# Optimization experiments

Hardware: AMD Instinct MI355X
Metric: run time of the kernel (lower is better)

Reference implementation:

```python
import jax, jax.numpy as jnp
import numpy as np

HIDDEN = 1024
GMM = 16


def setup_inputs() -> dict:
    key = jax.random.key(0)
    ks = jax.random.split(key, 9)
    B, T, D, S = 16, 1024, HIDDEN, 512
    sc_ih = 1.0 / np.sqrt(2 * D)
    sc_hh = 1.0 / np.sqrt(D)
    return {
        "input_h_c": jax.random.normal(ks[0], (B, T, D), jnp.float32),
        "memory": jax.random.normal(ks[1], (B, S, D), jnp.float32),
        "input_lengths": jax.random.randint(ks[2], (B,), 1, S + 1),
        "W_ih": jax.random.uniform(ks[3], (4 * D, 2 * D), jnp.float32, -sc_ih, sc_ih),
        "W_hh": jax.random.uniform(ks[4], (4 * D, D), jnp.float32, -sc_hh, sc_hh),
        "b_ih": jax.random.uniform(ks[5], (4 * D,), jnp.float32, -sc_hh, sc_hh),
        "b_hh": jax.random.uniform(ks[6], (4 * D,), jnp.float32, -sc_hh, sc_hh),
        "Wg_w": jax.random.uniform(ks[7], (3 * GMM, D), jnp.float32, -sc_hh, sc_hh),
        "Wg_b": jax.random.uniform(ks[8], (3 * GMM,), jnp.float32, -sc_hh, sc_hh),
    }


def reference(input_h_c, memory, input_lengths, W_ih, W_hh, b_ih, b_hh, Wg_w, Wg_b):
    B, T, D = input_h_c.shape
    S = memory.shape[1]
    M = Wg_b.shape[0] // 3
    b = b_ih + b_hh
    u = jnp.arange(S, dtype=input_h_c.dtype)  # positions u

    def step(carry, x_t):
        h, c, ctx = carry
        x = jnp.concatenate([x_t, ctx], axis=-1)  # [B, 2D]
        gates = x @ W_ih.T + h @ W_hh.T + b  # [B, 4D], torch gate order i,f,g,o
        i_g, f_g, g_g, o_g = jnp.split(gates, 4, axis=-1)
        c = jax.nn.sigmoid(f_g) * c + jax.nn.sigmoid(i_g) * jnp.tanh(g_g)
        h = jax.nn.sigmoid(o_g) * jnp.tanh(c)
        phi = h @ Wg_w.T + Wg_b  # [B, 3M]
        ksi = jnp.exp(phi[:, :M])
        beta = jnp.exp(phi[:, M:2 * M])
        alpha = jax.nn.softmax(phi[:, 2 * M:], axis=-1)
        # 1/(1+exp((ksi-u)/beta)) == sigmoid((u-ksi)/beta)
        z = (u[None, None, :] - ksi[:, :, None]) / beta[:, :, None]  # [B,M,S]
        half = 0.5 / beta[:, :, None]
        F_R = jax.nn.sigmoid(z + half)  # CDF at u+0.5
        F_L = jax.nn.sigmoid(z - half)  # CDF at u-0.5
        w = jnp.einsum('bm,bms->bs', alpha, F_R - F_L)  # [B,S]
        term = 1.0 - jnp.einsum('bm,bms->bs', alpha, F_R)  # [B,S]
        ctx = jnp.einsum('bs,bsd->bd', w, memory)  # [B,D]
        return (h, c, ctx), (w, term)

    h0 = jnp.zeros((B, D), input_h_c.dtype)
    c0 = jnp.zeros((B, D), input_h_c.dtype)
    ctx0 = jnp.zeros((B, D), input_h_c.dtype)
    (h, c, ctx), (ws, terms) = jax.lax.scan(
        step, (h0, c0, ctx0), jnp.swapaxes(input_h_c, 0, 1))
    alignment = jnp.swapaxes(ws, 0, 1)  # [B,T,S]
    term_last = terms[-1]  # [B,S]
    termination = jnp.take_along_axis(term_last, (input_lengths - 1)[:, None], axis=1)  # [B,1]
    context = ctx[:, None, :]  # [B,1,D], last-step context (as returned by torch forward)
    return (context, alignment, termination)
```

## Files before the change

kernel.cpp:

```cpp
#include <hip/hip_runtime.h>
#include <hip/hip_fp16.h>

#define BB 16
#define TT 1024
#define DD 1024
#define SS 512
#define KK 3072

#define NBLK 256
#define NTHR 512

#define OUT_ALIGN 16384
#define OUT_TERM  8404992

typedef __attribute__((ext_vector_type(8))) short short8;
typedef __attribute__((ext_vector_type(4))) float floatx4;
typedef __attribute__((ext_vector_type(2))) _Float16 half2v;

struct KParams {
  const float* x;
  const float* mem;
  const int*   lens;
  const float* W_ih;
  const float* W_hh;
  const float* b_ih;
  const float* b_hh;
  const float* Wg_w;
  const float* Wg_b;
  float* out;
  unsigned* bar;
  unsigned short* xc0;
  unsigned short* xc1;
  unsigned* wgbf;
};

__device__ __forceinline__ float sigf(float v) {
  return __builtin_amdgcn_rcpf(1.0f + __expf(-v));
}
__device__ __forceinline__ float tanhfast(float v) {
  float a = fabsf(v);
  float e = __expf(-2.0f * a);
  float r = (1.0f - e) * __builtin_amdgcn_rcpf(1.0f + e);
  return v < 0.0f ? -r : r;
}

__device__ __forceinline__ unsigned short f2bf(float f) {
  unsigned u = __float_as_uint(f);
  return (unsigned short)((u + 0x7FFFu + ((u >> 16) & 1u)) >> 16);
}
__device__ __forceinline__ float bf2f(unsigned short h) {
  return __uint_as_float(((unsigned)h) << 16);
}
__device__ __forceinline__ unsigned pack2bf(float a, float b) {
  return (unsigned)f2bf(a) | ((unsigned)f2bf(b) << 16);
}

__device__ __forceinline__ void cstore_u32(unsigned* p2, unsigned v) {
  __hip_atomic_store(p2, v, __ATOMIC_RELAXED, __HIP_MEMORY_SCOPE_AGENT);
}
__device__ __forceinline__ unsigned cload_u32(const unsigned* p2) {
  return __hip_atomic_load(p2, __ATOMIC_RELAXED, __HIP_MEMORY_SCOPE_AGENT);
}
__device__ __forceinline__ unsigned long long cload_u64(const unsigned long long* p2) {
  return __hip_atomic_load(p2, __ATOMIC_RELAXED, __HIP_MEMORY_SCOPE_AGENT);
}

__device__ __forceinline__ void lds_barrier() {
  asm volatile("s_waitcnt lgkmcnt(0)\n\ts_barrier" ::: "memory");
}

__device__ __forceinline__ void grid_barrier(unsigned* bar, unsigned ep, int blk) {
  __syncthreads();
  if (threadIdx.x == 0) cstore_u32(&bar[64 + blk * 32], ep);
  if (threadIdx.x < NBLK) {
    while (cload_u32(&bar[64 + threadIdx.x * 32]) < ep) __builtin_amdgcn_s_sleep(1);
  }
  __syncthreads();
}

union UF { unsigned long long u[2]; short8 s; };
struct AF8 { UF f[8]; };

__device__ __forceinline__ void xh_load(const unsigned short* xc, int ab, AF8& A) {
  const unsigned long long* xb = (const unsigned long long*)xc + ab;
#pragma unroll
  for (int s2 = 0; s2 < 4; ++s2) {
    A.f[s2].u[0]     = cload_u64(xb + s2 * 8);
    A.f[s2].u[1]     = cload_u64(xb + s2 * 8 + 1);
    A.f[4 + s2].u[0] = cload_u64(xb + 512 + s2 * 8);
    A.f[4 + s2].u[1] = cload_u64(xb + 512 + s2 * 8 + 1);
  }
}
__device__ __forceinline__ void xh_mfma(const AF8& A, const short8* bfr,
                                        floatx4& A0, floatx4& A1) {
  floatx4 a0 = {0.f, 0.f, 0.f, 0.f}, a1 = {0.f, 0.f, 0.f, 0.f};
#pragma unroll
  for (int s2 = 0; s2 < 4; s2 += 2) {
    a0 = __builtin_amdgcn_mfma_f32_16x16x32_bf16(A.f[s2].s,     bfr[s2],     a0, 0, 0, 0);
    a1 = __builtin_amdgcn_mfma_f32_16x16x32_bf16(A.f[s2 + 1].s, bfr[s2 + 1], a1, 0, 0, 0);
    a0 = __builtin_amdgcn_mfma_f32_16x16x32_bf16(A.f[4 + s2].s,     bfr[8 + s2],     a0, 0, 0, 0);
    a1 = __builtin_amdgcn_mfma_f32_16x16x32_bf16(A.f[4 + s2 + 1].s, bfr[8 + s2 + 1], a1, 0, 0, 0);
  }
  A0 = a0; A1 = a1;
}

__global__ __launch_bounds__(NTHR, 2) void tts_kernel(KParams p) {
  extern __shared__ char smem[];
  half2v* memsh2 = (half2v*)smem;

  __shared__ float redC[8 * 4 * 65 + 4];
  __shared__ unsigned hshu[8 * 65];
  __shared__ float php[384];
  __shared__ float alsh[16], ksish[16], invbsh[16];
  __shared__ float Rsh[513];
  __shared__ half2v wsh2[256];
  __shared__ float ctxp[8][64];
  __shared__ float bsh48[48];

  const int t    = threadIdx.x;
  const int blk  = blockIdx.x;
  const int lane = t & 63;
  const int w    = t >> 6;
  const int bbt  = blk & 15;
  const int dc   = blk >> 4;

  short8 bfr[12];
  {
    const int n = lane & 15;
    const int r = (n & 3) * 1024 + blk * 4 + (n >> 2);
    const int q = lane >> 4;
#pragma unroll
    for (int ki = 0; ki < 12; ++ki) {
      short8 v;
      const int k0 = (ki >> 2) * 1024 + w * 128 + (ki & 3) * 32 + q * 8;
#pragma unroll
      for (int j = 0; j < 8; ++j) {
        int k = k0 + j;
        float wv = (k < 2048) ? p.W_ih[(size_t)r * 2048 + k]
                              : p.W_hh[(size_t)r * 1024 + (k - 2048)];
        v[j] = (short)f2bf(wv);
      }
      bfr[ki] = v;
    }
  }
  float biasreg[4] = {0.f, 0.f, 0.f, 0.f};
  if (t < 64) {
    int dl = t & 3;
#pragma unroll
    for (int g = 0; g < 4; ++g) {
      int r = g * 1024 + blk * 4 + dl;
      biasreg[g] = p.b_ih[r] + p.b_hh[r];
    }
  }
  if (t < 48) bsh48[t] = p.Wg_b[t];
  {
    int dl = t & 63, sp = t >> 6;
    for (int pr = sp; pr < 256; pr += 8) {
      const float* mp = p.mem + (size_t)bbt * SS * DD + (size_t)(2 * pr) * DD + dc * 64 + dl;
      half2v v;
      v.x = (_Float16)mp[0];
      v.y = (_Float16)mp[DD];
      memsh2[pr * 64 + dl] = v;
    }
  }
  if (t < 32) {
    int k = dc * 64 + 2 * t;
    const float* xs = p.x + (size_t)bbt * TT * DD + k;
    cstore_u32((unsigned*)(p.xc0 + bbt * KK + k), pack2bf(xs[0], xs[1]));
    cstore_u32((unsigned*)(p.xc0 + bbt * KK + 1024 + k), 0u);
    cstore_u32((unsigned*)(p.xc0 + bbt * KK + 2048 + k), 0u);
  }
  if (blk == 0) {
    for (int i = t; i < 48 * 512; i += NTHR)
      cstore_u32(&p.wgbf[i], pack2bf(p.Wg_w[2 * i], p.Wg_w[2 * i + 1]));
  }

  float c_val = 0.0f;
  unsigned ep = 0;
  unsigned short* xc_cur = p.xc0;
  unsigned short* xc_nxt = p.xc1;
  const int ab = ((lane & 15) * KK + w * 128 + (lane >> 4) * 8) >> 2;

  grid_barrier(p.bar, ++ep, blk);

  floatx4 accXH0, accXH1;
  {
    AF8 a;
    xh_load(xc_cur, ab, a);
    xh_mfma(a, bfr, accXH0, accXH1);
  }

  for (int tstep = 0; tstep < TT; ++tstep) {
    {
      const unsigned long long* xb = (const unsigned long long*)xc_cur + ab;
      UF afc[4];
#pragma unroll
      for (int s2 = 0; s2 < 4; ++s2) {
        afc[s2].u[0] = cload_u64(xb + 256 + s2 * 8);
        afc[s2].u[1] = cload_u64(xb + 256 + s2 * 8 + 1);
      }
      floatx4 a0 = accXH0, a1 = accXH1;
      a0 = __builtin_amdgcn_mfma_f32_16x16x32_bf16(afc[0].s, bfr[4], a0, 0, 0, 0);
      a1 = __builtin_amdgcn_mfma_f32_16x16x32_bf16(afc[1].s, bfr[5], a1, 0, 0, 0);
      a0 = __builtin_amdgcn_mfma_f32_16x16x32_bf16(afc[2].s, bfr[6], a0, 0, 0, 0);
      a1 = __builtin_amdgcn_mfma_f32_16x16x32_bf16(afc[3].s, bfr[7], a1, 0, 0, 0);
      a0 += a1;
#pragma unroll
      for (int reg = 0; reg < 4; ++reg)
        redC[(w * 4 + reg) * 65 + lane] = a0[reg];
    }
    lds_barrier();
    if (t < 64) {
      int b = t >> 2, dl = t & 3;
      float gate[4];
#pragma unroll
      for (int g = 0; g < 4; ++g) {
        int ls = (b >> 2) * 16 + (dl * 4 + g);
        float s = biasreg[g];
#pragma unroll
        for (int w2 = 0; w2 < 8; ++w2) s += redC[(w2 * 4 + (b & 3)) * 65 + ls];
        gate[g] = s;
      }
      c_val = sigf(gate[1]) * c_val + sigf(gate[0]) * tanhfast(gate[2]);
      float hv = sigf(gate[3]) * tanhfast(c_val);
      float hn = __shfl_down(hv, 1, 64);
      if ((t & 1) == 0)
        cstore_u32((unsigned*)(xc_nxt + b * KK + 2048 + blk * 4 + dl), pack2bf(hv, hn));
    } else if (t < 96) {
      if (tstep + 1 < TT) {
        int k = dc * 64 + 2 * (t - 64);
        const float* xs = p.x + (size_t)bbt * TT * DD + (size_t)(tstep + 1) * DD + k;
        cstore_u32((unsigned*)(xc_nxt + bbt * KK + k), pack2bf(xs[0], xs[1]));
      }
    }
    grid_barrier(p.bar, ++ep, blk);

    unsigned hword = cload_u32((const unsigned*)(xc_nxt + bbt * KK + 2048) + t);
    AF8 afx;
    xh_load(xc_nxt, ab, afx);
    hshu[(t >> 6) * 65 + (t & 63)] = hword;
    lds_barrier();
    if (t < 384) {
      int m = t >> 3, part = t & 7;
      const unsigned* wgp = p.wgbf + m * 512 + part * 64;
      const unsigned* hrow = hshu + part * 65;
      float s0 = 0.f, s1 = 0.f, s2 = 0.f, s3 = 0.f;
#pragma unroll 4
      for (int i = 0; i < 64; i += 4) {
        unsigned u0 = hrow[i],     g0 = wgp[i];
        unsigned u1 = hrow[i + 1], g1 = wgp[i + 1];
        unsigned u2 = hrow[i + 2], g2 = wgp[i + 2];
        unsigned u3 = hrow[i + 3], g3 = wgp[i + 3];
        s0 += bf2f((unsigned short)u0) * bf2f((unsigned short)g0)
            + bf2f((unsigned short)(u0 >> 16)) * bf2f((unsigned short)(g0 >> 16));
        s1 += bf2f((unsigned short)u1) * bf2f((unsigned short)g1)
            + bf2f((unsigned short)(u1 >> 16)) * bf2f((unsigned short)(g1 >> 16));
        s2 += bf2f((unsigned short)u2) * bf2f((unsigned short)g2)
            + bf2f((unsigned short)(u2 >> 16)) * bf2f((unsigned short)(g2 >> 16));
        s3 += bf2f((unsigned short)u3) * bf2f((unsigned short)g3)
            + bf2f((unsigned short)(u3 >> 16)) * bf2f((unsigned short)(g3 >> 16));
      }
      php[t] = (s0 + s1) + (s2 + s3);
    }
    lds_barrier();
    if (t < 64) {
      float s = 0.f;
      if (t < 48) {
        s = bsh48[t];
#pragma unroll
        for (int i = 0; i < 8; ++i) s += php[t * 8 + i];
      }
      float mx = s;
#pragma unroll
      for (int o = 1; o < 16; o <<= 1) mx = fmaxf(mx, __shfl_xor(mx, o, 64));
      float e = __expf(s - mx);
      float sm = e;
#pragma unroll
      for (int o = 1; o < 16; o <<= 1) sm += __shfl_xor(sm, o, 64);
      float alpha_v = e * __builtin_amdgcn_rcpf(sm);
      float ksi_v   = __expf(s);
      float invb_v  = __expf(-s);
      if (t >= 32) { if (t < 48) alsh[t - 32] = alpha_v; }
      else if (t < 16) ksish[t] = ksi_v;
      else invbsh[t - 16] = invb_v;
      int m = t & 15;
      float am = __shfl(alpha_v, 32 + m, 64);
      float km = __shfl(ksi_v, m, 64);
      float bm = __shfl(invb_v, 16 + m, 64);
      float term = am * sigf((-0.5f - km) * bm);
#pragma unroll
      for (int o = 1; o < 16; o <<= 1) term += __shfl_xor(term, o, 64);
      if (t == 48) Rsh[0] = term;
    }
    lds_barrier();
    {
      float su = (float)t;
      float rv0 = 0.f, rv1 = 0.f;
#pragma unroll
      for (int m = 0; m < 16; m += 2) {
        rv0 += alsh[m]     * sigf((su + 0.5f - ksish[m])     * invbsh[m]);
        rv1 += alsh[m + 1] * sigf((su + 0.5f - ksish[m + 1]) * invbsh[m + 1]);
      }
      float rv = rv0 + rv1;
      float rvp = __shfl_up(rv, 1, 64);
      float rvn = __shfl_down(rv, 1, 64);
      Rsh[t + 1] = rv;
      if ((t & 1) == 0) {
        half2v v2;
        v2.x = (_Float16)(rv - rvp);
        v2.y = (_Float16)(rvn - rv);
        wsh2[t >> 1] = v2;
      }
      if (dc == 0 && (t & 63) != 0)
        p.out[OUT_ALIGN + ((size_t)bbt * TT + tstep) * SS + t] = rv - rvp;
    }
    lds_barrier();
    {
      if (dc == 0 && t < 8)
        p.out[OUT_ALIGN + ((size_t)bbt * TT + tstep) * SS + 64 * t] =
            Rsh[64 * t + 1] - Rsh[64 * t];
      if (tstep == TT - 1 && dc == 0 && t == 0)
        p.out[OUT_TERM + bbt] = 1.0f - Rsh[p.lens[bbt]];
      int dl = t & 63, sp = t >> 6;
      float b0 = Rsh[64 * sp], b1 = Rsh[64 * sp + 1], b2 = Rsh[64 * sp + 2];
      half2v w0;
      w0.x = (_Float16)(b1 - b0);
      w0.y = (_Float16)(b2 - b1);
      float s0 = __builtin_amdgcn_fdot2(memsh2[(sp * 32) * 64 + dl], w0, 0.f, false);
      float s1 = 0.f;
#pragma unroll
      for (int q = 1; q < 32; ++q) {
        int pr = sp * 32 + q;
        float v = __builtin_amdgcn_fdot2(memsh2[pr * 64 + dl], wsh2[pr],
                                         (q & 1) ? s1 : s0, false);
        if (q & 1) s1 = v; else s0 = v;
      }
      ctxp[sp][dl] = s0 + s1;
    }
    lds_barrier();
    if (t < 64) {
      float cv = 0.f;
#pragma unroll
      for (int pp = 0; pp < 8; ++pp) cv += ctxp[pp][t];
      if (tstep == TT - 1) p.out[bbt * DD + dc * 64 + t] = cv;
      float cvn = __shfl_down(cv, 1, 64);
      if ((t & 1) == 0)
        cstore_u32((unsigned*)(xc_nxt + bbt * KK + 1024 + dc * 64 + t), pack2bf(cv, cvn));
    }
    __builtin_amdgcn_sched_barrier(0);
    xh_mfma(afx, bfr, accXH0, accXH1);
    grid_barrier(p.bar, ++ep, blk);

    unsigned short* tmp = xc_cur; xc_cur = xc_nxt; xc_nxt = tmp;
  }
}

extern "C" void kernel_launch(void* const* d_in, const int* in_sizes, int n_in,
                              void* d_out, int out_size, void* d_ws, size_t ws_size,
                              hipStream_t stream) {
  (void)in_sizes; (void)n_in; (void)out_size; (void)ws_size;
  KParams p;
  p.x    = (const float*)d_in[0];
  p.mem  = (const float*)d_in[1];
  p.lens = (const int*)d_in[2];
  p.W_ih = (const float*)d_in[3];
  p.W_hh = (const float*)d_in[4];
  p.b_ih = (const float*)d_in[5];
  p.b_hh = (const float*)d_in[6];
  p.Wg_w = (const float*)d_in[7];
  p.Wg_b = (const float*)d_in[8];
  p.out  = (float*)d_out;
  p.bar  = (unsigned*)d_ws;
  p.xc0  = (unsigned short*)((char*)d_ws + 36864);
  p.xc1  = (unsigned short*)((char*)d_ws + 36864 + BB * KK * 2);
  p.wgbf = (unsigned*)((char*)d_ws + 36864 + 2 * BB * KK * 2);

  hipMemsetAsync(d_ws, 0, 36864, stream);

  const unsigned dynLds = 65536;
  hipFuncSetAttribute((const void*)tts_kernel, hipFuncAttributeMaxDynamicSharedMemorySize,
                      (int)dynLds);

  void* args[] = { &p };
  hipLaunchCooperativeKernel((const void*)tts_kernel, dim3(NBLK), dim3(NTHR), args, dynLds,
                             stream);
}
```

Measured before the change: 14.85 ms.

## Replace grid barriers with tagged per-word flag polling for X/H/C exchange

Removes the two per-step grid-wide barriers and instead packs each bf16 pair with a 32-bit step tag into a 64-bit word. Consumers poll the exact words they need until the tag matches, using double-buffered X/H/C arrays. The point is to let blocks proceed as soon as their inputs are ready instead of waiting on all 256 blocks. In exchange, global traffic doubles per exchanged element and spin polling is added on many loads. Buffer reuse across steps also depends on the tags for correctness.

```diff
diff --git a/kernel.cpp b/kernel.cpp
--- a/kernel.cpp
+++ b/kernel.cpp
@@ -5,7 +5,6 @@
 #define TT 1024
 #define DD 1024
 #define SS 512
-#define KK 3072
 
 #define NBLK 256
 #define NTHR 512
@@ -29,8 +28,9 @@
   const float* Wg_b;
   float* out;
   unsigned* bar;
-  unsigned short* xc0;
-  unsigned short* xc1;
+  unsigned long long* X;
+  unsigned long long* H;
+  unsigned long long* C;
   unsigned* wgbf;
 };
 
@@ -61,8 +61,14 @@
 __device__ __forceinline__ unsigned cload_u32(const unsigned* p2) {
   return __hip_atomic_load(p2, __ATOMIC_RELAXED, __HIP_MEMORY_SCOPE_AGENT);
 }
+__device__ __forceinline__ void cstore_u64(unsigned long long* p2, unsigned long long v) {
+  __hip_atomic_store(p2, v, __ATOMIC_RELAXED, __HIP_MEMORY_SCOPE_AGENT);
+}
 __device__ __forceinline__ unsigned long long cload_u64(const unsigned long long* p2) {
   return __hip_atomic_load(p2, __ATOMIC_RELAXED, __HIP_MEMORY_SCOPE_AGENT);
+}
+__device__ __forceinline__ unsigned long long tagpack(unsigned tag, unsigned data) {
+  return ((unsigned long long)tag << 32) | (unsigned long long)data;
 }
 
 __device__ __forceinline__ void lds_barrier() {
@@ -78,30 +84,28 @@
   __syncthreads();
 }
 
-union UF { unsigned long long u[2]; short8 s; };
-struct AF8 { UF f[8]; };
-
-__device__ __forceinline__ void xh_load(const unsigned short* xc, int ab, AF8& A) {
-  const unsigned long long* xb = (const unsigned long long*)xc + ab;
-#pragma unroll
-  for (int s2 = 0; s2 < 4; ++s2) {
-    A.f[s2].u[0]     = cload_u64(xb + s2 * 8);
-    A.f[s2].u[1]     = cload_u64(xb + s2 * 8 + 1);
-    A.f[4 + s2].u[0] = cload_u64(xb + 512 + s2 * 8);
-    A.f[4 + s2].u[1] = cload_u64(xb + 512 + s2 * 8 + 1);
-  }
-}
-__device__ __forceinline__ void xh_mfma(const AF8& A, const short8* bfr,
-                                        floatx4& A0, floatx4& A1) {
-  floatx4 a0 = {0.f, 0.f, 0.f, 0.f}, a1 = {0.f, 0.f, 0.f, 0.f};
-#pragma unroll
-  for (int s2 = 0; s2 < 4; s2 += 2) {
-    a0 = __builtin_amdgcn_mfma_f32_16x16x32_bf16(A.f[s2].s,     bfr[s2],     a0, 0, 0, 0);
-    a1 = __builtin_amdgcn_mfma_f32_16x16x32_bf16(A.f[s2 + 1].s, bfr[s2 + 1], a1, 0, 0, 0);
-    a0 = __builtin_amdgcn_mfma_f32_16x16x32_bf16(A.f[4 + s2].s,     bfr[8 + s2],     a0, 0, 0, 0);
-    a1 = __builtin_amdgcn_mfma_f32_16x16x32_bf16(A.f[4 + s2 + 1].s, bfr[8 + s2 + 1], a1, 0, 0, 0);
-  }
-  A0 = a0; A1 = a1;
+__device__ __forceinline__ void load16(const unsigned long long* b, unsigned long long* v) {
+#pragma unroll
+  for (int c = 0; c < 4; ++c)
+#pragma unroll
+    for (int j = 0; j < 4; ++j) v[c * 4 + j] = cload_u64(b + c * 16 + j);
+}
+__device__ __forceinline__ void poll16(const unsigned long long* b, unsigned long long* v,
+                                       unsigned want) {
+  for (;;) {
+    unsigned bad = 0;
+#pragma unroll
+    for (int i = 0; i < 16; ++i) bad |= ((unsigned)(v[i] >> 32)) ^ want;
+    if (!bad) return;
+    __builtin_amdgcn_s_sleep(1);
+    load16(b, v);
+  }
+}
+__device__ __forceinline__ short8 mk8(const unsigned long long* v) {
+  union { unsigned u[4]; short8 s; } pk;
+#pragma unroll
+  for (int j = 0; j < 4; ++j) pk.u[j] = (unsigned)v[j];
+  return pk.s;
 }
 
 __global__ __launch_bounds__(NTHR, 2) void tts_kernel(KParams p) {
@@ -164,46 +168,51 @@
     }
   }
   if (t < 32) {
-    int k = dc * 64 + 2 * t;
-    const float* xs = p.x + (size_t)bbt * TT * DD + k;
-    cstore_u32((unsigned*)(p.xc0 + bbt * KK + k), pack2bf(xs[0], xs[1]));
-    cstore_u32((unsigned*)(p.xc0 + bbt * KK + 1024 + k), 0u);
-    cstore_u32((unsigned*)(p.xc0 + bbt * KK + 2048 + k), 0u);
+    const float* xs = p.x + (size_t)bbt * TT * DD + dc * 64 + 2 * t;
+    cstore_u64(&p.X[bbt * 512 + dc * 32 + t], tagpack(1u, pack2bf(xs[0], xs[1])));
   }
   if (blk == 0) {
     for (int i = t; i < 48 * 512; i += NTHR)
       cstore_u32(&p.wgbf[i], pack2bf(p.Wg_w[2 * i], p.Wg_w[2 * i + 1]));
   }
+  grid_barrier(p.bar, 1u, blk);
 
   float c_val = 0.0f;
-  unsigned ep = 0;
-  unsigned short* xc_cur = p.xc0;
-  unsigned short* xc_nxt = p.xc1;
-  const int ab = ((lane & 15) * KK + w * 128 + (lane >> 4) * 8) >> 2;
-
-  grid_barrier(p.bar, ++ep, blk);
+  const int pab = (lane & 15) * 512 + w * 64 + (lane >> 4) * 4;
 
   floatx4 accXH0, accXH1;
   {
-    AF8 a;
-    xh_load(xc_cur, ab, a);
-    xh_mfma(a, bfr, accXH0, accXH1);
+    unsigned long long vx[16], vh[16];
+    const unsigned long long* xb = p.X + pab;
+    const unsigned long long* hb = p.H + 8192 + pab;
+    load16(xb, vx); load16(hb, vh);
+    poll16(xb, vx, 1u); poll16(hb, vh, 0u);
+    floatx4 b0 = {0.f,0.f,0.f,0.f}, b1 = {0.f,0.f,0.f,0.f};
+    b0 = __builtin_amdgcn_mfma_f32_16x16x32_bf16(mk8(vx + 0),  bfr[0],  b0, 0, 0, 0);
+    b1 = __builtin_amdgcn_mfma_f32_16x16x32_bf16(mk8(vx + 4),  bfr[1],  b1, 0, 0, 0);
+    b0 = __builtin_amdgcn_mfma_f32_16x16x32_bf16(mk8(vx + 8),  bfr[2],  b0, 0, 0, 0);
+    b1 = __builtin_amdgcn_mfma_f32_16x16x32_bf16(mk8(vx + 12), bfr[3],  b1, 0, 0, 0);
+    b0 = __builtin_amdgcn_mfma_f32_16x16x32_bf16(mk8(vh + 0),  bfr[8],  b0, 0, 0, 0);
+    b1 = __builtin_amdgcn_mfma_f32_16x16x32_bf16(mk8(vh + 4),  bfr[9],  b1, 0, 0, 0);
+    b0 = __builtin_amdgcn_mfma_f32_16x16x32_bf16(mk8(vh + 8),  bfr[10], b0, 0, 0, 0);
+    b1 = __builtin_amdgcn_mfma_f32_16x16x32_bf16(mk8(vh + 12), bfr[11], b1, 0, 0, 0);
+    accXH0 = b0; accXH1 = b1;
   }
 
   for (int tstep = 0; tstep < TT; ++tstep) {
+    const int q1 = tstep & 1;
+    const int q0 = q1 ^ 1;
+
     {
-      const unsigned long long* xb = (const unsigned long long*)xc_cur + ab;
-      UF afc[4];
-#pragma unroll
-      for (int s2 = 0; s2 < 4; ++s2) {
-        afc[s2].u[0] = cload_u64(xb + 256 + s2 * 8);
-        afc[s2].u[1] = cload_u64(xb + 256 + s2 * 8 + 1);
-      }
+      const unsigned long long* cb = p.C + q0 * 8192 + pab;
+      unsigned long long vc[16];
+      load16(cb, vc);
+      poll16(cb, vc, (unsigned)tstep);
       floatx4 a0 = accXH0, a1 = accXH1;
-      a0 = __builtin_amdgcn_mfma_f32_16x16x32_bf16(afc[0].s, bfr[4], a0, 0, 0, 0);
-      a1 = __builtin_amdgcn_mfma_f32_16x16x32_bf16(afc[1].s, bfr[5], a1, 0, 0, 0);
-      a0 = __builtin_amdgcn_mfma_f32_16x16x32_bf16(afc[2].s, bfr[6], a0, 0, 0, 0);
-      a1 = __builtin_amdgcn_mfma_f32_16x16x32_bf16(afc[3].s, bfr[7], a1, 0, 0, 0);
+      a0 = __builtin_amdgcn_mfma_f32_16x16x32_bf16(mk8(vc + 0),  bfr[4], a0, 0, 0, 0);
+      a1 = __builtin_amdgcn_mfma_f32_16x16x32_bf16(mk8(vc + 4),  bfr[5], a1, 0, 0, 0);
+      a0 = __builtin_amdgcn_mfma_f32_16x16x32_bf16(mk8(vc + 8),  bfr[6], a0, 0, 0, 0);
+      a1 = __builtin_amdgcn_mfma_f32_16x16x32_bf16(mk8(vc + 12), bfr[7], a1, 0, 0, 0);
       a0 += a1;
 #pragma unroll
       for (int reg = 0; reg < 4; ++reg)
@@ -224,21 +233,34 @@
       c_val = sigf(gate[1]) * c_val + sigf(gate[0]) * tanhfast(gate[2]);
       float hv = sigf(gate[3]) * tanhfast(c_val);
       float hn = __shfl_down(hv, 1, 64);
-      if ((t & 1) == 0)
-        cstore_u32((unsigned*)(xc_nxt + b * KK + 2048 + blk * 4 + dl), pack2bf(hv, hn));
+      if ((dl & 1) == 0)
+        cstore_u64(&p.H[q1 * 8192 + b * 512 + blk * 2 + (dl >> 1)],
+                   tagpack((unsigned)(tstep + 1), pack2bf(hv, hn)));
     } else if (t < 96) {
       if (tstep + 1 < TT) {
-        int k = dc * 64 + 2 * (t - 64);
-        const float* xs = p.x + (size_t)bbt * TT * DD + (size_t)(tstep + 1) * DD + k;
-        cstore_u32((unsigned*)(xc_nxt + bbt * KK + k), pack2bf(xs[0], xs[1]));
-      }
-    }
-    grid_barrier(p.bar, ++ep, blk);
-
-    unsigned hword = cload_u32((const unsigned*)(xc_nxt + bbt * KK + 2048) + t);
-    AF8 afx;
-    xh_load(xc_nxt, ab, afx);
-    hshu[(t >> 6) * 65 + (t & 63)] = hword;
+        const float* xs = p.x + (size_t)bbt * TT * DD + (size_t)(tstep + 1) * DD +
+                          dc * 64 + 2 * (t - 64);
+        cstore_u64(&p.X[q0 * 8192 + bbt * 512 + dc * 32 + (t - 64)],
+                   tagpack((unsigned)(tstep + 2), pack2bf(xs[0], xs[1])));
+      }
+    }
+
+    const unsigned wantH = (unsigned)(tstep + 1);
+    unsigned long long vx[16], vh[16];
+    const unsigned long long* xb = p.X + q0 * 8192 + pab;
+    const unsigned long long* hb = p.H + q1 * 8192 + pab;
+    if (tstep + 1 < TT) { load16(xb, vx); load16(hb, vh); }
+    __builtin_amdgcn_sched_barrier(0);
+    unsigned long long hv64;
+    {
+      const unsigned long long* hp = p.H + q1 * 8192 + bbt * 512 + t;
+      hv64 = cload_u64(hp);
+      while ((unsigned)(hv64 >> 32) != wantH) {
+        __builtin_amdgcn_s_sleep(1);
+        hv64 = cload_u64(hp);
+      }
+    }
+    hshu[(t >> 6) * 65 + (t & 63)] = (unsigned)hv64;
     lds_barrier();
     if (t < 384) {
       int m = t >> 3, part = t & 7;
@@ -345,13 +367,24 @@
       if (tstep == TT - 1) p.out[bbt * DD + dc * 64 + t] = cv;
       float cvn = __shfl_down(cv, 1, 64);
       if ((t & 1) == 0)
-        cstore_u32((unsigned*)(xc_nxt + bbt * KK + 1024 + dc * 64 + t), pack2bf(cv, cvn));
-    }
-    __builtin_amdgcn_sched_barrier(0);
-    xh_mfma(afx, bfr, accXH0, accXH1);
-    grid_barrier(p.bar, ++ep, blk);
-
-    unsigned short* tmp = xc_cur; xc_cur = xc_nxt; xc_nxt = tmp;
+        cstore_u64(&p.C[q1 * 8192 + bbt * 512 + dc * 32 + (t >> 1)],
+                   tagpack((unsigned)(tstep + 1), pack2bf(cv, cvn)));
+    }
+    if (tstep + 1 < TT) {
+      poll16(xb, vx, (unsigned)(tstep + 2));
+      poll16(hb, vh, wantH);
+      __builtin_amdgcn_sched_barrier(0);
+      floatx4 b0 = {0.f,0.f,0.f,0.f}, b1 = {0.f,0.f,0.f,0.f};
+      b0 = __builtin_amdgcn_mfma_f32_16x16x32_bf16(mk8(vx + 0),  bfr[0],  b0, 0, 0, 0);
+      b1 = __builtin_amdgcn_mfma_f32_16x16x32_bf16(mk8(vx + 4),  bfr[1],  b1, 0, 0, 0);
+      b0 = __builtin_amdgcn_mfma_f32_16x16x32_bf16(mk8(vx + 8),  bfr[2],  b0, 0, 0, 0);
+      b1 = __builtin_amdgcn_mfma_f32_16x16x32_bf16(mk8(vx + 12), bfr[3],  b1, 0, 0, 0);
+      b0 = __builtin_amdgcn_mfma_f32_16x16x32_bf16(mk8(vh + 0),  bfr[8],  b0, 0, 0, 0);
+      b1 = __builtin_amdgcn_mfma_f32_16x16x32_bf16(mk8(vh + 4),  bfr[9],  b1, 0, 0, 0);
+      b0 = __builtin_amdgcn_mfma_f32_16x16x32_bf16(mk8(vh + 8),  bfr[10], b0, 0, 0, 0);
+      b1 = __builtin_amdgcn_mfma_f32_16x16x32_bf16(mk8(vh + 12), bfr[11], b1, 0, 0, 0);
+      accXH0 = b0; accXH1 = b1;
+    }
   }
 }
 
@@ -371,11 +404,12 @@
   p.Wg_b = (const float*)d_in[8];
   p.out  = (float*)d_out;
   p.bar  = (unsigned*)d_ws;
-  p.xc0  = (unsigned short*)((char*)d_ws + 36864);
-  p.xc1  = (unsigned short*)((char*)d_ws + 36864 + BB * KK * 2);
-  p.wgbf = (unsigned*)((char*)d_ws + 36864 + 2 * BB * KK * 2);
-
-  hipMemsetAsync(d_ws, 0, 36864, stream);
+  p.X    = (unsigned long long*)((char*)d_ws + 36864);
+  p.H    = (unsigned long long*)((char*)d_ws + 36864 + 131072);
+  p.C    = (unsigned long long*)((char*)d_ws + 36864 + 262144);
+  p.wgbf = (unsigned*)((char*)d_ws + 36864 + 393216);
+
+  hipMemsetAsync(d_ws, 0, 36864 + 393216, stream);
 
   const unsigned dynLds = 65536;
   hipFuncSetAttribute((const void*)tts_kernel, hipFuncAttributeMaxDynamicSharedMemorySize,
```

New measurement: 25.01 ms. 1.68x slower.

## Halve block count, double per-block tile, read x directly from global

Applied to the files above, without the earlier changes.

Reduces the cooperative grid from 256 to 128 blocks. Each block now owns 8 hidden units (two N-tiles of MFMA) and 128 context columns, with twice the memory slice in LDS (128KB dynamic). The input x is no longer staged through the shared bf16 exchange buffer. Each wave loads it straight from global memory and converts it with v_cvt_pk_bf16_f32, which shrinks the exchange buffer to ctx+h. The grid barrier polling is adapted to 128 blocks. The goal is lower grid-barrier and cross-block traffic cost per timestep, at the price of more per-block work, register pressure and LDS use.

```diff
diff --git a/kernel.cpp b/kernel.cpp
--- a/kernel.cpp
+++ b/kernel.cpp
@@ -5,9 +5,9 @@
 #define TT 1024
 #define DD 1024
 #define SS 512
-#define KK 3072
-
-#define NBLK 256
+#define KK2 2048
+
+#define NBLK 128
 #define NTHR 512
 
 #define OUT_ALIGN 16384
@@ -54,6 +54,11 @@
 __device__ __forceinline__ unsigned pack2bf(float a, float b) {
   return (unsigned)f2bf(a) | ((unsigned)f2bf(b) << 16);
 }
+__device__ __forceinline__ unsigned cvtpk(float a, float b) {
+  unsigned r;
+  asm volatile("v_cvt_pk_bf16_f32 %0, %1, %2" : "=v"(r) : "v"(a), "v"(b));
+  return r;
+}
 
 __device__ __forceinline__ void cstore_u32(unsigned* p2, unsigned v) {
   __hip_atomic_store(p2, v, __ATOMIC_RELAXED, __HIP_MEMORY_SCOPE_AGENT);
@@ -72,49 +77,43 @@
 __device__ __forceinline__ void grid_barrier(unsigned* bar, unsigned ep, int blk) {
   __syncthreads();
   if (threadIdx.x == 0) cstore_u32(&bar[64 + blk * 32], ep);
-  if (threadIdx.x < NBLK) {
-    while (cload_u32(&bar[64 + threadIdx.x * 32]) < ep) __builtin_amdgcn_s_sleep(1);
+  if (threadIdx.x < 64) {
+    while (cload_u32(&bar[64 + (int)threadIdx.x * 32]) < ep) __builtin_amdgcn_s_sleep(1);
+    while (cload_u32(&bar[64 + ((int)threadIdx.x + 64) * 32]) < ep) __builtin_amdgcn_s_sleep(1);
   }
   __syncthreads();
 }
 
-union UF { unsigned long long u[2]; short8 s; };
-struct AF8 { UF f[8]; };
-
-__device__ __forceinline__ void xh_load(const unsigned short* xc, int ab, AF8& A) {
-  const unsigned long long* xb = (const unsigned long long*)xc + ab;
-#pragma unroll
-  for (int s2 = 0; s2 < 4; ++s2) {
-    A.f[s2].u[0]     = cload_u64(xb + s2 * 8);
-    A.f[s2].u[1]     = cload_u64(xb + s2 * 8 + 1);
-    A.f[4 + s2].u[0] = cload_u64(xb + 512 + s2 * 8);
-    A.f[4 + s2].u[1] = cload_u64(xb + 512 + s2 * 8 + 1);
-  }
-}
-__device__ __forceinline__ void xh_mfma(const AF8& A, const short8* bfr,
-                                        floatx4& A0, floatx4& A1) {
-  floatx4 a0 = {0.f, 0.f, 0.f, 0.f}, a1 = {0.f, 0.f, 0.f, 0.f};
-#pragma unroll
-  for (int s2 = 0; s2 < 4; s2 += 2) {
-    a0 = __builtin_amdgcn_mfma_f32_16x16x32_bf16(A.f[s2].s,     bfr[s2],     a0, 0, 0, 0);
-    a1 = __builtin_amdgcn_mfma_f32_16x16x32_bf16(A.f[s2 + 1].s, bfr[s2 + 1], a1, 0, 0, 0);
-    a0 = __builtin_amdgcn_mfma_f32_16x16x32_bf16(A.f[4 + s2].s,     bfr[8 + s2],     a0, 0, 0, 0);
-    a1 = __builtin_amdgcn_mfma_f32_16x16x32_bf16(A.f[4 + s2 + 1].s, bfr[8 + s2 + 1], a1, 0, 0, 0);
-  }
-  A0 = a0; A1 = a1;
+union UF { unsigned w[4]; unsigned long long u[2]; short8 s; };
+
+#define MFMA16 __builtin_amdgcn_mfma_f32_16x16x32_bf16
+
+__device__ __forceinline__ void xh_mfma(const UF* xf, const UF* hf, const short8* bfr,
+                                        floatx4& a00, floatx4& a01,
+                                        floatx4& a10, floatx4& a11) {
+  floatx4 z = {0.f, 0.f, 0.f, 0.f};
+  a00 = z; a01 = z; a10 = z; a11 = z;
+  a00 = MFMA16(xf[0].s, bfr[0],  a00, 0, 0, 0); a01 = MFMA16(xf[1].s, bfr[1],  a01, 0, 0, 0);
+  a10 = MFMA16(xf[0].s, bfr[12], a10, 0, 0, 0); a11 = MFMA16(xf[1].s, bfr[13], a11, 0, 0, 0);
+  a00 = MFMA16(xf[2].s, bfr[2],  a00, 0, 0, 0); a01 = MFMA16(xf[3].s, bfr[3],  a01, 0, 0, 0);
+  a10 = MFMA16(xf[2].s, bfr[14], a10, 0, 0, 0); a11 = MFMA16(xf[3].s, bfr[15], a11, 0, 0, 0);
+  a00 = MFMA16(hf[0].s, bfr[8],  a00, 0, 0, 0); a01 = MFMA16(hf[1].s, bfr[9],  a01, 0, 0, 0);
+  a10 = MFMA16(hf[0].s, bfr[20], a10, 0, 0, 0); a11 = MFMA16(hf[1].s, bfr[21], a11, 0, 0, 0);
+  a00 = MFMA16(hf[2].s, bfr[10], a00, 0, 0, 0); a01 = MFMA16(hf[3].s, bfr[11], a01, 0, 0, 0);
+  a10 = MFMA16(hf[2].s, bfr[22], a10, 0, 0, 0); a11 = MFMA16(hf[3].s, bfr[23], a11, 0, 0, 0);
 }
 
 __global__ __launch_bounds__(NTHR, 2) void tts_kernel(KParams p) {
   extern __shared__ char smem[];
   half2v* memsh2 = (half2v*)smem;
 
-  __shared__ float redC[8 * 4 * 65 + 4];
+  __shared__ float redC[64 * 65 + 4];
   __shared__ unsigned hshu[8 * 65];
   __shared__ float php[384];
   __shared__ float alsh[16], ksish[16], invbsh[16];
   __shared__ float Rsh[513];
   __shared__ half2v wsh2[256];
-  __shared__ float ctxp[8][64];
+  __shared__ float ctxp[4][128];
   __shared__ float bsh48[48];
 
   const int t    = threadIdx.x;
@@ -124,121 +123,145 @@
   const int bbt  = blk & 15;
   const int dc   = blk >> 4;
 
-  short8 bfr[12];
+  short8 bfr[24];
   {
     const int n = lane & 15;
-    const int r = (n & 3) * 1024 + blk * 4 + (n >> 2);
     const int q = lane >> 4;
 #pragma unroll
-    for (int ki = 0; ki < 12; ++ki) {
-      short8 v;
-      const int k0 = (ki >> 2) * 1024 + w * 128 + (ki & 3) * 32 + q * 8;
-#pragma unroll
-      for (int j = 0; j < 8; ++j) {
-        int k = k0 + j;
-        float wv = (k < 2048) ? p.W_ih[(size_t)r * 2048 + k]
-                              : p.W_hh[(size_t)r * 1024 + (k - 2048)];
-        v[j] = (short)f2bf(wv);
-      }
-      bfr[ki] = v;
+    for (int nt = 0; nt < 2; ++nt) {
+      const int r = (n & 3) * 1024 + blk * 8 + nt * 4 + (n >> 2);
+#pragma unroll
+      for (int ki = 0; ki < 12; ++ki) {
+        short8 v;
+        const int k0 = (ki >> 2) * 1024 + w * 128 + (ki & 3) * 32 + q * 8;
+#pragma unroll
+        for (int j = 0; j < 8; ++j) {
+          int k = k0 + j;
+          float wv = (k < 2048) ? p.W_ih[(size_t)r * 2048 + k]
+                                : p.W_hh[(size_t)r * 1024 + (k - 2048)];
+          v[j] = (short)f2bf(wv);
+        }
+        bfr[nt * 12 + ki] = v;
+      }
     }
   }
   float biasreg[4] = {0.f, 0.f, 0.f, 0.f};
-  if (t < 64) {
-    int dl = t & 3;
+  if (t < 128) {
+    int dl = t & 7;
 #pragma unroll
     for (int g = 0; g < 4; ++g) {
-      int r = g * 1024 + blk * 4 + dl;
+      int r = g * 1024 + blk * 8 + dl;
       biasreg[g] = p.b_ih[r] + p.b_hh[r];
     }
   }
   if (t < 48) bsh48[t] = p.Wg_b[t];
   {
-    int dl = t & 63, sp = t >> 6;
-    for (int pr = sp; pr < 256; pr += 8) {
-      const float* mp = p.mem + (size_t)bbt * SS * DD + (size_t)(2 * pr) * DD + dc * 64 + dl;
+    int dl = t & 127, sp = t >> 7;
+    for (int pr = sp; pr < 256; pr += 4) {
+      const float* mp = p.mem + (size_t)bbt * SS * DD + (size_t)(2 * pr) * DD + dc * 128 + dl;
       half2v v;
       v.x = (_Float16)mp[0];
       v.y = (_Float16)mp[DD];
-      memsh2[pr * 64 + dl] = v;
-    }
-  }
-  if (t < 32) {
-    int k = dc * 64 + 2 * t;
-    const float* xs = p.x + (size_t)bbt * TT * DD + k;
-    cstore_u32((unsigned*)(p.xc0 + bbt * KK + k), pack2bf(xs[0], xs[1]));
-    cstore_u32((unsigned*)(p.xc0 + bbt * KK + 1024 + k), 0u);
-    cstore_u32((unsigned*)(p.xc0 + bbt * KK + 2048 + k), 0u);
+      memsh2[pr * 128 + dl] = v;
+    }
   }
   if (blk == 0) {
     for (int i = t; i < 48 * 512; i += NTHR)
       cstore_u32(&p.wgbf[i], pack2bf(p.Wg_w[2 * i], p.Wg_w[2 * i + 1]));
   }
+  grid_barrier(p.bar, 1u, blk);
 
   float c_val = 0.0f;
-  unsigned ep = 0;
+  unsigned ep = 1;
   unsigned short* xc_cur = p.xc0;
   unsigned short* xc_nxt = p.xc1;
-  const int ab = ((lane & 15) * KK + w * 128 + (lane >> 4) * 8) >> 2;
-
-  grid_barrier(p.bar, ++ep, blk);
-
-  floatx4 accXH0, accXH1;
+  const int ab2 = ((lane & 15) * KK2 + w * 128 + ((lane >> 4) * 8)) >> 2;
+  const float* xrow = p.x + (size_t)(lane & 15) * TT * DD + w * 128 + ((lane >> 4) * 8);
+
+  floatx4 acc00, acc01, acc10, acc11;
   {
-    AF8 a;
-    xh_load(xc_cur, ab, a);
-    xh_mfma(a, bfr, accXH0, accXH1);
+    UF xf[4], hf[4];
+#pragma unroll
+    for (int sub = 0; sub < 4; ++sub) {
+      floatx4 lo = *(const floatx4*)(xrow + sub * 32);
+      floatx4 hi = *(const floatx4*)(xrow + sub * 32 + 4);
+      xf[sub].w[0] = cvtpk(lo[0], lo[1]); xf[sub].w[1] = cvtpk(lo[2], lo[3]);
+      xf[sub].w[2] = cvtpk(hi[0], hi[1]); xf[sub].w[3] = cvtpk(hi[2], hi[3]);
+    }
+    const unsigned long long* hb = (const unsigned long long*)p.xc0 + ab2 + 256;
+#pragma unroll
+    for (int sub = 0; sub < 4; ++sub) {
+      hf[sub].u[0] = cload_u64(hb + sub * 8);
+      hf[sub].u[1] = cload_u64(hb + sub * 8 + 1);
+    }
+    xh_mfma(xf, hf, bfr, acc00, acc01, acc10, acc11);
   }
 
   for (int tstep = 0; tstep < TT; ++tstep) {
     {
-      const unsigned long long* xb = (const unsigned long long*)xc_cur + ab;
-      UF afc[4];
-#pragma unroll
-      for (int s2 = 0; s2 < 4; ++s2) {
-        afc[s2].u[0] = cload_u64(xb + 256 + s2 * 8);
-        afc[s2].u[1] = cload_u64(xb + 256 + s2 * 8 + 1);
-      }
-      floatx4 a0 = accXH0, a1 = accXH1;
-      a0 = __builtin_amdgcn_mfma_f32_16x16x32_bf16(afc[0].s, bfr[4], a0, 0, 0, 0);
-      a1 = __builtin_amdgcn_mfma_f32_16x16x32_bf16(afc[1].s, bfr[5], a1, 0, 0, 0);
-      a0 = __builtin_amdgcn_mfma_f32_16x16x32_bf16(afc[2].s, bfr[6], a0, 0, 0, 0);
-      a1 = __builtin_amdgcn_mfma_f32_16x16x32_bf16(afc[3].s, bfr[7], a1, 0, 0, 0);
-      a0 += a1;
-#pragma unroll
-      for (int reg = 0; reg < 4; ++reg)
-        redC[(w * 4 + reg) * 65 + lane] = a0[reg];
-    }
-    lds_barrier();
-    if (t < 64) {
-      int b = t >> 2, dl = t & 3;
+      const unsigned long long* cb = (const unsigned long long*)xc_cur + ab2;
+      UF fc[4];
+#pragma unroll
+      for (int sub = 0; sub < 4; ++sub) {
+        fc[sub].u[0] = cload_u64(cb + sub * 8);
+        fc[sub].u[1] = cload_u64(cb + sub * 8 + 1);
+      }
+      floatx4 c00 = acc00, c01 = acc01, c10 = acc10, c11 = acc11;
+      c00 = MFMA16(fc[0].s, bfr[4],  c00, 0, 0, 0); c01 = MFMA16(fc[1].s, bfr[5],  c01, 0, 0, 0);
+      c10 = MFMA16(fc[0].s, bfr[16], c10, 0, 0, 0); c11 = MFMA16(fc[1].s, bfr[17], c11, 0, 0, 0);
+      c00 = MFMA16(fc[2].s, bfr[6],  c00, 0, 0, 0); c01 = MFMA16(fc[3].s, bfr[7],  c01, 0, 0, 0);
+      c10 = MFMA16(fc[2].s, bfr[18], c10, 0, 0, 0); c11 = MFMA16(fc[3].s, bfr[19], c11, 0, 0, 0);
+      c00 += c01; c10 += c11;
+#pragma unroll
+      for (int reg = 0; reg < 4; ++reg) {
+        redC[(w * 8 + reg) * 65 + lane]     = c00[reg];
+        redC[(w * 8 + 4 + reg) * 65 + lane] = c10[reg];
+      }
+    }
+    lds_barrier();
+    if (t < 128) {
+      int b = t >> 3, dl = t & 7, nt = dl >> 2, dl4 = dl & 3;
+      int row = nt * 4 + (b & 3);
       float gate[4];
 #pragma unroll
       for (int g = 0; g < 4; ++g) {
-        int ls = (b >> 2) * 16 + (dl * 4 + g);
+        int ls = ((b >> 2) << 4) | (dl4 * 4 + g);
         float s = biasreg[g];
 #pragma unroll
-        for (int w2 = 0; w2 < 8; ++w2) s += redC[(w2 * 4 + (b & 3)) * 65 + ls];
+        for (int w2 = 0; w2 < 8; ++w2) s += redC[(w2 * 8 + row) * 65 + ls];
         gate[g] = s;
       }
       c_val = sigf(gate[1]) * c_val + sigf(gate[0]) * tanhfast(gate[2]);
       float hv = sigf(gate[3]) * tanhfast(c_val);
       float hn = __shfl_down(hv, 1, 64);
       if ((t & 1) == 0)
-        cstore_u32((unsigned*)(xc_nxt + b * KK + 2048 + blk * 4 + dl), pack2bf(hv, hn));
-    } else if (t < 96) {
-      if (tstep + 1 < TT) {
-        int k = dc * 64 + 2 * (t - 64);
-        const float* xs = p.x + (size_t)bbt * TT * DD + (size_t)(tstep + 1) * DD + k;
-        cstore_u32((unsigned*)(xc_nxt + bbt * KK + k), pack2bf(xs[0], xs[1]));
-      }
+        cstore_u32((unsigned*)(xc_nxt + b * KK2 + 1024 + blk * 8 + dl), pack2bf(hv, hn));
     }
     grid_barrier(p.bar, ++ep, blk);
 
-    unsigned hword = cload_u32((const unsigned*)(xc_nxt + bbt * KK + 2048) + t);
-    AF8 afx;
-    xh_load(xc_nxt, ab, afx);
-    hshu[(t >> 6) * 65 + (t & 63)] = hword;
+    unsigned long long hword = 0;
+    if (t < 256) hword = cload_u64((const unsigned long long*)xc_nxt + bbt * 512 + 256 + t);
+    UF hf[4];
+    floatx4 xlo[4], xhi[4];
+    if (tstep + 1 < TT) {
+      const unsigned long long* hb = (const unsigned long long*)xc_nxt + ab2 + 256;
+#pragma unroll
+      for (int sub = 0; sub < 4; ++sub) {
+        hf[sub].u[0] = cload_u64(hb + sub * 8);
+        hf[sub].u[1] = cload_u64(hb + sub * 8 + 1);
+      }
+      const float* xp = xrow + (size_t)(tstep + 1) * DD;
+#pragma unroll
+      for (int sub = 0; sub < 4; ++sub) {
+        xlo[sub] = *(const floatx4*)(xp + sub * 32);
+        xhi[sub] = *(const floatx4*)(xp + sub * 32 + 4);
+      }
+    }
+    if (t < 256) {
+      int row = t >> 5, col = (t & 31) * 2;
+      hshu[row * 65 + col]     = (unsigned)hword;
+      hshu[row * 65 + col + 1] = (unsigned)(hword >> 32);
+    }
     lds_barrier();
     if (t < 384) {
       int m = t >> 3, part = t & 7;
@@ -321,34 +344,39 @@
             Rsh[64 * t + 1] - Rsh[64 * t];
       if (tstep == TT - 1 && dc == 0 && t == 0)
         p.out[OUT_TERM + bbt] = 1.0f - Rsh[p.lens[bbt]];
-      int dl = t & 63, sp = t >> 6;
-      float b0 = Rsh[64 * sp], b1 = Rsh[64 * sp + 1], b2 = Rsh[64 * sp + 2];
-      half2v w0;
-      w0.x = (_Float16)(b1 - b0);
-      w0.y = (_Float16)(b2 - b1);
-      float s0 = __builtin_amdgcn_fdot2(memsh2[(sp * 32) * 64 + dl], w0, 0.f, false);
-      float s1 = 0.f;
-#pragma unroll
+      int dl = t & 127, sp = t >> 7;
+      const int pb = sp * 64;
+      half2v wa = wsh2[pb];       wa.x = (_Float16)(Rsh[2 * pb + 1] - Rsh[2 * pb]);
+      half2v wb = wsh2[pb + 32];  wb.x = (_Float16)(Rsh[2 * pb + 65] - Rsh[2 * pb + 64]);
+      float s0 = __builtin_amdgcn_fdot2(memsh2[pb * 128 + dl], wa, 0.f, false);
+      float s1 = __builtin_amdgcn_fdot2(memsh2[(pb + 32) * 128 + dl], wb, 0.f, false);
+#pragma unroll 8
       for (int q = 1; q < 32; ++q) {
-        int pr = sp * 32 + q;
-        float v = __builtin_amdgcn_fdot2(memsh2[pr * 64 + dl], wsh2[pr],
-                                         (q & 1) ? s1 : s0, false);
-        if (q & 1) s1 = v; else s0 = v;
+        s0 = __builtin_amdgcn_fdot2(memsh2[(pb + q) * 128 + dl],      wsh2[pb + q],      s0, false);
+        s1 = __builtin_amdgcn_fdot2(memsh2[(pb + 32 + q) * 128 + dl], wsh2[pb + 32 + q], s1, false);
       }
       ctxp[sp][dl] = s0 + s1;
     }
     lds_barrier();
-    if (t < 64) {
-      float cv = 0.f;
-#pragma unroll
-      for (int pp = 0; pp < 8; ++pp) cv += ctxp[pp][t];
-      if (tstep == TT - 1) p.out[bbt * DD + dc * 64 + t] = cv;
+    if (t < 128) {
+      float cv = ctxp[0][t] + ctxp[1][t] + ctxp[2][t] + ctxp[3][t];
+      if (tstep == TT - 1) p.out[bbt * DD + dc * 128 + t] = cv;
       float cvn = __shfl_down(cv, 1, 64);
       if ((t & 1) == 0)
-        cstore_u32((unsigned*)(xc_nxt + bbt * KK + 1024 + dc * 64 + t), pack2bf(cv, cvn));
+        cstore_u32((unsigned*)(xc_nxt + bbt * KK2 + dc * 128 + t), pack2bf(cv, cvn));
     }
     __builtin_amdgcn_sched_barrier(0);
-    xh_mfma(afx, bfr, accXH0, accXH1);
+    if (tstep + 1 < TT) {
+      UF xf[4];
+#pragma unroll
+      for (int sub = 0; sub < 4; ++sub) {
+        xf[sub].w[0] = cvtpk(xlo[sub][0], xlo[sub][1]);
+        xf[sub].w[1] = cvtpk(xlo[sub][2], xlo[sub][3]);
+        xf[sub].w[2] = cvtpk(xhi[sub][0], xhi[sub][1]);
+        xf[sub].w[3] = cvtpk(xhi[sub][2], xhi[sub][3]);
+      }
+      xh_mfma(xf, hf, bfr, acc00, acc01, acc10, acc11);
+    }
     grid_barrier(p.bar, ++ep, blk);
 
     unsigned short* tmp = xc_cur; xc_cur = xc_nxt; xc_nxt = tmp;
@@ -372,12 +400,12 @@
   p.out  = (float*)d_out;
   p.bar  = (unsigned*)d_ws;
   p.xc0  = (unsigned short*)((char*)d_ws + 36864);
-  p.xc1  = (unsigned short*)((char*)d_ws + 36864 + BB * KK * 2);
-  p.wgbf = (unsigned*)((char*)d_ws + 36864 + 2 * BB * KK * 2);
-
-  hipMemsetAsync(d_ws, 0, 36864, stream);
-
-  const unsigned dynLds = 65536;
+  p.xc1  = (unsigned short*)((char*)d_ws + 36864 + 65536);
+  p.wgbf = (unsigned*)((char*)d_ws + 36864 + 131072);
+
+  hipMemsetAsync(d_ws, 0, 36864 + 65536, stream);
+
+  const unsigned dynLds = 131072;
   hipFuncSetAttribute((const void*)tts_kernel, hipFuncAttributeMaxDynamicSharedMemorySize,
                       (int)dynLds);
 
```

Result: slower. 16.19 ms (+9.0%).
